# Optimization experiments

Measured on AMD Instinct MI355X. Metric: run time of the kernel, lower is better.

The kernel has to match this reference:

```python
import jax, jax.numpy as jnp
import numpy as np

DRN = 0.4
TWO_PI = 2.0 * np.pi


def _mlp(x, ws, bs):
    # torch_geometric MLP with act='LeakyRelu' (slope 0.01), dropout=0 (eval), norm treated as identity (eval running stats)
    for w, b in zip(ws[:-1], bs[:-1]):
        x = jax.nn.leaky_relu(x @ w + b, 0.01)
    return x @ ws[-1] + bs[-1]


def _conv(x, ws, bs):
    # x: [B, N, F] = [pt, h..., ang_re, ang_im]. Dense masked equivalent of radius-graph EdgeConv.
    ang = x[..., -2:]
    d2 = jnp.sum((ang[:, :, None, :] - ang[:, None, :, :]) ** 2, -1)
    adj = (d2 <= DRN * DRN).astype(x.dtype)  # [B,N,N], i=target, j=source, self-loops included (radius ball)
    h = x[..., 1:-2]
    B, N, H = h.shape
    hi = jnp.broadcast_to(h[:, :, None, :], (B, N, N, H))
    hj = jnp.broadcast_to(h[:, None, :, :], (B, N, N, H))
    re, im = ang[..., 0], ang[..., 1]
    r2 = re * re + im * im
    nrm = jnp.maximum(jnp.sqrt(r2[:, :, None] * r2[:, None, :]), 1e-12)
    cos = (re[:, :, None] * re[:, None, :] + im[:, :, None] * im[:, None, :]) / nrm
    sin = (im[:, :, None] * re[:, None, :] - re[:, :, None] * im[:, None, :]) / nrm
    feat = jnp.concatenate([hi, hj, hj - hi, cos[..., None], sin[..., None]], -1)
    m = _mlp(feat, ws, bs)  # [B,N,N,H_out+1]
    # pt-weighted aggregation: message pt is the TARGET's pt (x_i[:, :1] in torch code)
    pt = x[..., 0]
    msg_pt = pt[:, :, None] * adj
    denom = jnp.sum(msg_pt, -1, keepdims=True)
    w = jnp.where(denom > 0, msg_pt / denom, 0.0)  # nan_to_num equivalent
    agg = jnp.einsum('bij,bijk->bik', w, m)
    sw = jnp.sum(w, -1)
    agg_pt = pt * sw                      # sum_j w * pt_i
    agg_ang = ang * sw[..., None]          # sum_j w * ang_i
    # phase renormalization: exp(2*pi*i*gamma) * (re + i*im)
    gamma = agg[..., -1]
    c, s = jnp.cos(TWO_PI * gamma), jnp.sin(TWO_PI * gamma)
    re2 = c * agg_ang[..., 0] - s * agg_ang[..., 1]
    im2 = s * agg_ang[..., 0] + c * agg_ang[..., 1]
    return jnp.concatenate([agg_pt[..., None], agg[..., :-1], re2[..., None], im2[..., None]], -1)


def _forward(pt, angles, c0w, c0b, c1w, c1b, rw, rb):
    absz = jnp.sqrt(jnp.sum(angles ** 2, -1))  # |view_as_complex(angles)|
    x = jnp.concatenate([pt[..., None], absz[..., None], angles], -1)
    x = _conv(x, c0w, c0b)
    x = _conv(x, c1w, c1b)
    # pt-weighted readout over particles
    ptf = x[..., 0]
    denom = jnp.sum(ptf, -1, keepdims=True)
    wj = jnp.where(denom > 0, ptf / denom, 0.0)
    xg = jnp.einsum('bn,bnf->bf', wj, x[..., 1:])
    logits = _mlp(xg[:, :-2], rw, rb)
    return jnp.concatenate([jax.nn.sigmoid(logits), xg[:, -2:]], -1)


def setup_inputs() -> dict:
    key = jax.random.key(0)
    ks = jax.random.split(key, 16)
    B, N = 128, 128
    pt = jax.random.uniform(ks[0], (B, N), jnp.float32, 0.05, 1.0)  # all > 0 so mask is all-true
    angles = 0.25 * jax.random.normal(ks[1], (B, N, 2), jnp.float32)

    def lin(k, i, o):
        return (0.2 / np.sqrt(i)) * jax.random.normal(k, (i, o), jnp.float32) * np.sqrt(i)

    H = 16
    return {
        'pt': pt, 'angles': angles,
        'c0_w0': lin(ks[2], 5, H), 'c0_b0': jnp.zeros((H,), jnp.float32),
        'c0_w1': lin(ks[3], H, H + 1), 'c0_b1': jnp.zeros((H + 1,), jnp.float32),
        'c1_w0': lin(ks[4], 3 * H + 2, H), 'c1_b0': jnp.zeros((H,), jnp.float32),
        'c1_w1': lin(ks[5], H, H + 1), 'c1_b1': jnp.zeros((H + 1,), jnp.float32),
        'r_w0': lin(ks[6], H, 32), 'r_b0': jnp.zeros((32,), jnp.float32),
        'r_w1': lin(ks[7], 32, 32), 'r_b1': jnp.zeros((32,), jnp.float32),
        'r_w2': lin(ks[8], 32, 1), 'r_b2': jnp.zeros((1,), jnp.float32),
    }


def reference(pt, angles, c0_w0, c0_b0, c0_w1, c0_b1, c1_w0, c1_b0, c1_w1, c1_b1, r_w0, r_b0, r_w1, r_b1, r_w2, r_b2):
    return _forward(pt, angles, (c0_w0, c0_w1), (c0_b0, c0_b1), (c1_w0, c1_w1), (c1_b0, c1_b1), (r_w0, r_w1, r_w2), (r_b0, r_b1, r_b2))
```

## Files before the change

### kernel.cpp

```cpp
#include <hip/hip_runtime.h>
#include <math.h>


#define BB 128
#define NN 128
#define BN (BB * NN)

typedef float f32x2 __attribute__((ext_vector_type(2)));

__device__ __forceinline__ f32x2 pk2(float s) { f32x2 r; r[0] = s; r[1] = s; return r; }
__device__ __forceinline__ f32x2 pkfma(f32x2 a, f32x2 b, f32x2 c) {
    return __builtin_elementwise_fma(a, b, c);
}
__device__ __forceinline__ f32x2 pkmax(f32x2 a, f32x2 b) {
    return __builtin_elementwise_max(a, b);
}

template <int CTRL>
__device__ __forceinline__ float dpp_add(float x) {
    int tmp = __builtin_amdgcn_update_dpp(0, __float_as_int(x), CTRL, 0xF, 0xF, true);
    return x + __int_as_float(tmp);
}

__device__ __forceinline__ float grp16_sum(float x) {
    x = dpp_add<0xB1>(x);
    x = dpp_add<0x4E>(x);
    x = dpp_add<0x114>(x);
    x = dpp_add<0x118>(x);
    return x;
}

__device__ __forceinline__ float bcast_grp(float x, int bidx) {
    return __int_as_float(__builtin_amdgcn_ds_bpermute(bidx, __float_as_int(x)));
}

__global__ __launch_bounds__(256) void conv0_kernel(
    const float* __restrict__ ang,
    const float* __restrict__ w0,
    const float* __restrict__ b0,
    const float* __restrict__ w1,
    const float* __restrict__ b1,
    const float* __restrict__ nw0,
    const float* __restrict__ nb0,
    float* __restrict__ ang1,
    float* __restrict__ u1,
    float* __restrict__ v1)
{
    const int tid  = threadIdx.x;
    const int lane = tid & 63;
    const int wid  = tid >> 6;
    const int t    = lane & 15;
    const int g    = lane >> 4;
    const int ni   = blockIdx.x * 16 + wid * 4 + g;
    const int base = (blockIdx.x >> 3) << 7;

    __shared__ float hls[16][17];

    const float2 ai = ((const float2*)ang)[ni];
    const float r2i = fmaf(ai.x, ai.x, ai.y * ai.y);
    const float abszi = __builtin_amdgcn_sqrtf(r2i);
    const float invi  = __builtin_amdgcn_rsqf(r2i);

    f32x2 u0b2[8], q02[8], wc2[8], ws2[8];
    #pragma unroll
    for (int p = 0; p < 8; ++p) {
        f32x2 wa  = *(const f32x2*)(w0 + 2 * p);
        f32x2 wb  = *(const f32x2*)(w0 + 16 + 2 * p);
        f32x2 wcv = *(const f32x2*)(w0 + 32 + 2 * p);
        f32x2 bb  = *(const f32x2*)(b0 + 2 * p);
        u0b2[p] = pkfma(pk2(abszi), wa - wcv, bb);
        q02[p]  = wb + wcv;
        wc2[p]  = *(const f32x2*)(w0 + 48 + 2 * p);
        ws2[p]  = *(const f32x2*)(w0 + 64 + 2 * p);
    }

    float w1row[16], w1g[16];
    #pragma unroll
    for (int k = 0; k < 16; ++k) {
        w1row[k] = w1[k * 17 + t];
        w1g[k]   = w1[k * 17 + 16];
    }
    const float b1t = b1[t], b1g = b1[16];

    const int o   = lane & 31;
    const int kk  = o & 15;
    const bool isU = (o < 16);
    float wk[16];
    {
        const int off = isU ? 0 : 256;
        #pragma unroll
        for (int c = 0; c < 16; ++c) {
            float a_ = nw0[off + c * 16 + kk];
            float c_ = nw0[512 + c * 16 + kk];
            wk[c] = isU ? (a_ - c_) : (a_ + c_);
        }
    }
    const float accb = isU ? nb0[kk] : 0.0f;

    f32x2 A2[8];
    #pragma unroll
    for (int p = 0; p < 8; ++p) A2[p] = pk2(0.0f);
    float degf = 0.0f;

    #pragma unroll 4
    for (int jj = 0; jj < 8; ++jj) {
        const float2 aj = ((const float2*)ang)[base + jj * 16 + t];
        const float r2j = fmaf(aj.x, aj.x, aj.y * aj.y);
        const float abszj = __builtin_amdgcn_sqrtf(r2j);
        const float ivj   = __builtin_amdgcn_rsqf(r2j);
        const float dre = ai.x - aj.x, dim = ai.y - aj.y;
        const float d2 = fmaf(dre, dre, dim * dim);
        const float adjf = (d2 <= 0.16f) ? 1.0f : 0.0f;
        degf += adjf;
        const float inv = fminf(invi * ivj, 1e12f);
        const f32x2 cos2 = pk2(fmaf(ai.x, aj.x, ai.y * aj.y) * inv);
        const f32x2 sin2 = pk2(fmaf(ai.y, aj.x, -(ai.x * aj.y)) * inv);
        const f32x2 ab2 = pk2(abszj);
        const f32x2 adj2 = pk2(adjf);
        #pragma unroll
        for (int p = 0; p < 8; ++p) {
            f32x2 z = pkfma(ab2, q02[p], u0b2[p]);
            z = pkfma(cos2, wc2[p], z);
            z = pkfma(sin2, ws2[p], z);
            f32x2 a = pkmax(z, z * 0.01f);
            A2[p] = pkfma(a, adj2, A2[p]);
        }
    }

    const int bidx = (lane | 15) << 2;
    float Ak[16];
    #pragma unroll
    for (int p = 0; p < 8; ++p) {
        Ak[2 * p]     = bcast_grp(grp16_sum(A2[p][0]), bidx);
        Ak[2 * p + 1] = bcast_grp(grp16_sum(A2[p][1]), bidx);
    }
    const float degA = bcast_grp(grp16_sum(degf), bidx);
    const float invdeg = __builtin_amdgcn_rcpf(degA);

    float s = 0.0f, sg = 0.0f;
    #pragma unroll
    for (int k = 0; k < 16; ++k) {
        s  = fmaf(Ak[k], w1row[k], s);
        sg = fmaf(Ak[k], w1g[k], sg);
    }
    const float mt    = fmaf(s, invdeg, b1t);
    const float gamma = fmaf(sg, invdeg, b1g);

    {
        const float gf = gamma - floorf(gamma);
        const float cs = __builtin_amdgcn_cosf(gf);
        const float sn = __builtin_amdgcn_sinf(gf);
        const float re2 = cs * ai.x - sn * ai.y;
        const float im2 = fmaf(sn, ai.x, cs * ai.y);
        if (t == 0) ((float4*)ang1)[ni] = make_float4(re2, im2, invi, 0.0f);
    }

    hls[wid * 4 + g][t] = mt;

    #pragma unroll
    for (int p = 0; p < 2; ++p) {
        const int nl = (lane >> 5) + 2 * p;
        const int node = wid * 4 + nl;
        float acc = accb;
        #pragma unroll
        for (int c = 0; c < 16; ++c) acc = fmaf(hls[node][c], wk[c], acc);
        const int nig = blockIdx.x * 16 + nl;
        const int nout = (blockIdx.x * 16 + node);
        (void)nig;
        if (isU) u1[nout * 16 + kk] = acc;
        else     v1[nout * 16 + kk] = acc;
    }
}

__global__ __launch_bounds__(256) void conv1_kernel(
    const float* __restrict__ pt,
    const float* __restrict__ ang1,
    const float* __restrict__ u1,
    const float* __restrict__ v1,
    const float* __restrict__ w0,
    const float* __restrict__ w1,
    const float* __restrict__ b1,
    float* __restrict__ part)
{
    const int tid  = threadIdx.x;
    const int lane = tid & 63;
    const int wid  = tid >> 6;
    const int t    = lane & 15;
    const int g    = lane >> 4;
    const int ni   = blockIdx.x * 16 + wid * 4 + g;
    const int base = (blockIdx.x >> 3) << 7;

    const float4 a4 = ((const float4*)ang1)[ni];
    const float rei = a4.x, imi = a4.y, invi = a4.z;
    const float ptf = pt[ni];

    f32x2 u0b2[8], wc2[8], ws2[8];
    {
        const float4* ug = (const float4*)(u1 + (size_t)ni * 16);
        float4 q0 = ug[0], q1 = ug[1], q2 = ug[2], q3 = ug[3];
        u0b2[0][0] = q0.x; u0b2[0][1] = q0.y; u0b2[1][0] = q0.z; u0b2[1][1] = q0.w;
        u0b2[2][0] = q1.x; u0b2[2][1] = q1.y; u0b2[3][0] = q1.z; u0b2[3][1] = q1.w;
        u0b2[4][0] = q2.x; u0b2[4][1] = q2.y; u0b2[5][0] = q2.z; u0b2[5][1] = q2.w;
        u0b2[6][0] = q3.x; u0b2[6][1] = q3.y; u0b2[7][0] = q3.z; u0b2[7][1] = q3.w;
    }
    #pragma unroll
    for (int p = 0; p < 8; ++p) {
        wc2[p] = *(const f32x2*)(w0 + 768 + 2 * p);
        ws2[p] = *(const f32x2*)(w0 + 784 + 2 * p);
    }

    float w1row[16], w1g[16];
    #pragma unroll
    for (int k = 0; k < 16; ++k) {
        w1row[k] = w1[k * 17 + t];
        w1g[k]   = w1[k * 17 + 16];
    }
    const float b1t = b1[t], b1g = b1[16];

    f32x2 A2[8];
    #pragma unroll
    for (int p = 0; p < 8; ++p) A2[p] = pk2(0.0f);
    float degf = 0.0f;

    #pragma unroll 4
    for (int jj = 0; jj < 8; ++jj) {
        const int j = base + jj * 16 + t;
        const float4 aj = ((const float4*)ang1)[j];
        f32x2 vj2[8];
        {
            const float4* vg = (const float4*)(v1 + (size_t)j * 16);
            float4 q0 = vg[0], q1 = vg[1], q2 = vg[2], q3 = vg[3];
            vj2[0][0] = q0.x; vj2[0][1] = q0.y; vj2[1][0] = q0.z; vj2[1][1] = q0.w;
            vj2[2][0] = q1.x; vj2[2][1] = q1.y; vj2[3][0] = q1.z; vj2[3][1] = q1.w;
            vj2[4][0] = q2.x; vj2[4][1] = q2.y; vj2[5][0] = q2.z; vj2[5][1] = q2.w;
            vj2[6][0] = q3.x; vj2[6][1] = q3.y; vj2[7][0] = q3.z; vj2[7][1] = q3.w;
        }
        const float dre = rei - aj.x, dim = imi - aj.y;
        const float d2 = fmaf(dre, dre, dim * dim);
        const float adjf = (d2 <= 0.16f) ? 1.0f : 0.0f;
        degf += adjf;
        const float inv = fminf(invi * aj.z, 1e12f);
        const f32x2 cos2 = pk2(fmaf(rei, aj.x, imi * aj.y) * inv);
        const f32x2 sin2 = pk2(fmaf(imi, aj.x, -(rei * aj.y)) * inv);
        const f32x2 adj2 = pk2(adjf);
        #pragma unroll
        for (int p = 0; p < 8; ++p) {
            f32x2 z = u0b2[p] + vj2[p];
            z = pkfma(cos2, wc2[p], z);
            z = pkfma(sin2, ws2[p], z);
            f32x2 a = pkmax(z, z * 0.01f);
            A2[p] = pkfma(a, adj2, A2[p]);
        }
    }

    const int bidx = (lane | 15) << 2;
    float Ak[16];
    #pragma unroll
    for (int p = 0; p < 8; ++p) {
        Ak[2 * p]     = bcast_grp(grp16_sum(A2[p][0]), bidx);
        Ak[2 * p + 1] = bcast_grp(grp16_sum(A2[p][1]), bidx);
    }
    const float degA = bcast_grp(grp16_sum(degf), bidx);
    const float invdeg = __builtin_amdgcn_rcpf(degA);

    float s = 0.0f, sg = 0.0f;
    #pragma unroll
    for (int k = 0; k < 16; ++k) {
        s  = fmaf(Ak[k], w1row[k], s);
        sg = fmaf(Ak[k], w1g[k], sg);
    }
    const float mt    = fmaf(s, invdeg, b1t);
    const float gamma = fmaf(sg, invdeg, b1g);

    const float gf = gamma - floorf(gamma);
    const float cs = __builtin_amdgcn_cosf(gf);
    const float sn = __builtin_amdgcn_sinf(gf);
    const float re2 = cs * rei - sn * imi;
    const float im2 = fmaf(sn, rei, cs * imi);

    float pm  = ptf * mt;
    float pre = ptf * re2;
    float pim = ptf * im2;
    float ppt = ptf;
    pm  += __int_as_float(__builtin_amdgcn_ds_swizzle(__float_as_int(pm),  0x401F));
    pre += __int_as_float(__builtin_amdgcn_ds_swizzle(__float_as_int(pre), 0x401F));
    pim += __int_as_float(__builtin_amdgcn_ds_swizzle(__float_as_int(pim), 0x401F));
    ppt += __int_as_float(__builtin_amdgcn_ds_swizzle(__float_as_int(ppt), 0x401F));
    pm  += __shfl_xor(pm, 32);
    pre += __shfl_xor(pre, 32);
    pim += __shfl_xor(pim, 32);
    ppt += __shfl_xor(ppt, 32);

    float* po = part + (size_t)(blockIdx.x * 4 + wid) * 20;
    if (lane < 16)       po[lane] = pm;
    else if (lane == 16) po[16] = pre;
    else if (lane == 17) po[17] = pim;
    else if (lane == 18) po[18] = ppt;
}

__global__ __launch_bounds__(64) void readout_kernel(
    const float* __restrict__ part,
    const float* __restrict__ w0, const float* __restrict__ b0,
    const float* __restrict__ w1, const float* __restrict__ b1,
    const float* __restrict__ w2, const float* __restrict__ b2,
    float* __restrict__ out) {
    const int b = blockIdx.x;
    const int t = threadIdx.x;

    __shared__ float sbuf[19];
    __shared__ float xg[18];
    __shared__ float h1r[32];

    if (t < 19) {
        float s0 = 0.0f, s1 = 0.0f, s2 = 0.0f, s3 = 0.0f;
        const float* pb = part + (size_t)b * 32 * 20 + t;
        #pragma unroll
        for (int r = 0; r < 32; r += 4) {
            s0 += pb[(r + 0) * 20];
            s1 += pb[(r + 1) * 20];
            s2 += pb[(r + 2) * 20];
            s3 += pb[(r + 3) * 20];
        }
        sbuf[t] = (s0 + s1) + (s2 + s3);
    }
    const float invd = __builtin_amdgcn_rcpf(sbuf[18]);
    if (t < 18) xg[t] = sbuf[t] * invd;

    if (t < 32) {
        float h = b0[t];
        #pragma unroll
        for (int k = 0; k < 16; ++k) h = fmaf(xg[k], w0[k * 32 + t], h);
        h = fmaxf(h, 0.01f * h);
        h1r[t] = h;
    }
    if (t < 32) {
        float h = b1[t];
        #pragma unroll
        for (int k = 0; k < 32; ++k) h = fmaf(h1r[k], w1[k * 32 + t], h);
        h = fmaxf(h, 0.01f * h);
        float p = h * w2[t];
        #pragma unroll
        for (int off = 16; off; off >>= 1) p += __shfl_xor(p, off);
        if (t == 0) {
            out[b * 3 + 0] = 1.0f / (1.0f + expf(-(p + b2[0])));
            out[b * 3 + 1] = xg[16];
            out[b * 3 + 2] = xg[17];
        }
    }
}

extern "C" void kernel_launch(void* const* d_in, const int* in_sizes, int n_in,
                              void* d_out, int out_size, void* d_ws, size_t ws_size,
                              hipStream_t stream) {
    const float* pt    = (const float*)d_in[0];
    const float* ang   = (const float*)d_in[1];
    const float* c0_w0 = (const float*)d_in[2];
    const float* c0_b0 = (const float*)d_in[3];
    const float* c0_w1 = (const float*)d_in[4];
    const float* c0_b1 = (const float*)d_in[5];
    const float* c1_w0 = (const float*)d_in[6];
    const float* c1_b0 = (const float*)d_in[7];
    const float* c1_w1 = (const float*)d_in[8];
    const float* c1_b1 = (const float*)d_in[9];
    const float* r_w0  = (const float*)d_in[10];
    const float* r_b0  = (const float*)d_in[11];
    const float* r_w1  = (const float*)d_in[12];
    const float* r_b1  = (const float*)d_in[13];
    const float* r_w2  = (const float*)d_in[14];
    const float* r_b2  = (const float*)d_in[15];
    float* out = (float*)d_out;
    float* ws = (float*)d_ws;

    float* ang1  = ws;
    float* u1    = ang1 + (size_t)BN * 4;
    float* v1    = u1 + (size_t)BN * 16;
    float* partb = v1 + (size_t)BN * 16;

    hipLaunchKernelGGL(conv0_kernel, dim3(BN / 16), dim3(256), 0, stream,
                       ang, c0_w0, c0_b0, c0_w1, c0_b1, c1_w0, c1_b0,
                       ang1, u1, v1);
    hipLaunchKernelGGL(conv1_kernel, dim3(BN / 16), dim3(256), 0, stream,
                       pt, ang1, u1, v1, c1_w0, c1_w1, c1_b1, partb);
    hipLaunchKernelGGL(readout_kernel, dim3(BB), dim3(64), 0, stream,
                       partb, r_w0, r_b0, r_w1, r_b1, r_w2, r_b2, out);
}
```

Before: 30.21 us.

## Prefetch neighbour loads, store unit vectors, pack FMAs, add occupancy bounds

Conv0 now loads all neighbour angles up front and fully unrolls its loop. It stores normalised unit vectors (rotated by the phase) so conv1 computes cos/sin directly without the per-edge inverse-norm multiply. Conv1 software-pipelines the neighbour record and v1 loads three steps ahead, and both kernels defer weight loads, use packed FMAs for the final matvecs, and set launch_bounds min-blocks to 4. This trades register pressure and a slight change in rounding for better latency hiding and fewer ALU ops.

```diff
diff --git a/kernel.cpp b/kernel.cpp
--- a/kernel.cpp
+++ b/kernel.cpp
@@ -34,7 +34,14 @@
     return __int_as_float(__builtin_amdgcn_ds_bpermute(bidx, __float_as_int(x)));
 }
 
-__global__ __launch_bounds__(256) void conv0_kernel(
+__device__ __forceinline__ f32x2 grp16_red2(f32x2 x, int bidx) {
+    f32x2 r;
+    r[0] = bcast_grp(grp16_sum(x[0]), bidx);
+    r[1] = bcast_grp(grp16_sum(x[1]), bidx);
+    return r;
+}
+
+__global__ __launch_bounds__(256, 4) void conv0_kernel(
     const float* __restrict__ ang,
     const float* __restrict__ w0,
     const float* __restrict__ b0,
@@ -42,24 +49,29 @@
     const float* __restrict__ b1,
     const float* __restrict__ nw0,
     const float* __restrict__ nb0,
-    float* __restrict__ ang1,
+    float* __restrict__ rec,
     float* __restrict__ u1,
     float* __restrict__ v1)
 {
-    const int tid  = threadIdx.x;
-    const int lane = tid & 63;
-    const int wid  = tid >> 6;
+    const int lane = threadIdx.x & 63;
+    const int wid  = threadIdx.x >> 6;
     const int t    = lane & 15;
     const int g    = lane >> 4;
     const int ni   = blockIdx.x * 16 + wid * 4 + g;
     const int base = (blockIdx.x >> 3) << 7;
 
-    __shared__ float hls[16][17];
+    __shared__ float hls[16][20];
 
     const float2 ai = ((const float2*)ang)[ni];
     const float r2i = fmaf(ai.x, ai.x, ai.y * ai.y);
     const float abszi = __builtin_amdgcn_sqrtf(r2i);
-    const float invi  = __builtin_amdgcn_rsqf(r2i);
+    const float ivi = fminf(__builtin_amdgcn_rsqf(r2i), 1e12f);
+    const float eix = ai.x * ivi, eiy = ai.y * ivi;
+
+    float2 ajv[8];
+    #pragma unroll
+    for (int jj = 0; jj < 8; ++jj)
+        ajv[jj] = ((const float2*)ang)[base + jj * 16 + t];
 
     f32x2 u0b2[8], q02[8], wc2[8], ws2[8];
     #pragma unroll
@@ -74,47 +86,24 @@
         ws2[p]  = *(const f32x2*)(w0 + 64 + 2 * p);
     }
 
-    float w1row[16], w1g[16];
-    #pragma unroll
-    for (int k = 0; k < 16; ++k) {
-        w1row[k] = w1[k * 17 + t];
-        w1g[k]   = w1[k * 17 + 16];
-    }
-    const float b1t = b1[t], b1g = b1[16];
-
-    const int o   = lane & 31;
-    const int kk  = o & 15;
-    const bool isU = (o < 16);
-    float wk[16];
-    {
-        const int off = isU ? 0 : 256;
-        #pragma unroll
-        for (int c = 0; c < 16; ++c) {
-            float a_ = nw0[off + c * 16 + kk];
-            float c_ = nw0[512 + c * 16 + kk];
-            wk[c] = isU ? (a_ - c_) : (a_ + c_);
-        }
-    }
-    const float accb = isU ? nb0[kk] : 0.0f;
-
     f32x2 A2[8];
     #pragma unroll
     for (int p = 0; p < 8; ++p) A2[p] = pk2(0.0f);
     float degf = 0.0f;
 
-    #pragma unroll 4
+    #pragma unroll
     for (int jj = 0; jj < 8; ++jj) {
-        const float2 aj = ((const float2*)ang)[base + jj * 16 + t];
+        const float2 aj = ajv[jj];
         const float r2j = fmaf(aj.x, aj.x, aj.y * aj.y);
         const float abszj = __builtin_amdgcn_sqrtf(r2j);
-        const float ivj   = __builtin_amdgcn_rsqf(r2j);
+        const float ivj = fminf(__builtin_amdgcn_rsqf(r2j), 1e12f);
+        const float ejx = aj.x * ivj, ejy = aj.y * ivj;
         const float dre = ai.x - aj.x, dim = ai.y - aj.y;
         const float d2 = fmaf(dre, dre, dim * dim);
         const float adjf = (d2 <= 0.16f) ? 1.0f : 0.0f;
         degf += adjf;
-        const float inv = fminf(invi * ivj, 1e12f);
-        const f32x2 cos2 = pk2(fmaf(ai.x, aj.x, ai.y * aj.y) * inv);
-        const f32x2 sin2 = pk2(fmaf(ai.y, aj.x, -(ai.x * aj.y)) * inv);
+        const f32x2 cos2 = pk2(fmaf(eix, ejx, eiy * ejy));
+        const f32x2 sin2 = pk2(fmaf(eiy, ejx, -(eix * ejy)));
         const f32x2 ab2 = pk2(abszj);
         const f32x2 adj2 = pk2(adjf);
         #pragma unroll
@@ -128,53 +117,76 @@
     }
 
     const int bidx = (lane | 15) << 2;
-    float Ak[16];
+    f32x2 Ak2[8];
+    #pragma unroll
+    for (int p = 0; p < 8; ++p) Ak2[p] = grp16_red2(A2[p], bidx);
+    const float invdeg = __builtin_amdgcn_rcpf(bcast_grp(grp16_sum(degf), bidx));
+
+    f32x2 s2 = pk2(0.0f), g2 = pk2(0.0f);
     #pragma unroll
     for (int p = 0; p < 8; ++p) {
-        Ak[2 * p]     = bcast_grp(grp16_sum(A2[p][0]), bidx);
-        Ak[2 * p + 1] = bcast_grp(grp16_sum(A2[p][1]), bidx);
-    }
-    const float degA = bcast_grp(grp16_sum(degf), bidx);
-    const float invdeg = __builtin_amdgcn_rcpf(degA);
-
-    float s = 0.0f, sg = 0.0f;
-    #pragma unroll
-    for (int k = 0; k < 16; ++k) {
-        s  = fmaf(Ak[k], w1row[k], s);
-        sg = fmaf(Ak[k], w1g[k], sg);
-    }
-    const float mt    = fmaf(s, invdeg, b1t);
-    const float gamma = fmaf(sg, invdeg, b1g);
+        f32x2 wr; wr[0] = w1[(2 * p) * 17 + t];  wr[1] = w1[(2 * p + 1) * 17 + t];
+        f32x2 wg; wg[0] = w1[(2 * p) * 17 + 16]; wg[1] = w1[(2 * p + 1) * 17 + 16];
+        s2 = pkfma(Ak2[p], wr, s2);
+        g2 = pkfma(Ak2[p], wg, g2);
+    }
+    const float mt    = fmaf(s2[0] + s2[1], invdeg, b1[t]);
+    const float gamma = fmaf(g2[0] + g2[1], invdeg, b1[16]);
 
     {
         const float gf = gamma - floorf(gamma);
         const float cs = __builtin_amdgcn_cosf(gf);
         const float sn = __builtin_amdgcn_sinf(gf);
-        const float re2 = cs * ai.x - sn * ai.y;
-        const float im2 = fmaf(sn, ai.x, cs * ai.y);
-        if (t == 0) ((float4*)ang1)[ni] = make_float4(re2, im2, invi, 0.0f);
+        if (t == 0) {
+            const float re2 = cs * ai.x - sn * ai.y;
+            const float im2 = fmaf(sn, ai.x, cs * ai.y);
+            const float e1x = cs * eix - sn * eiy;
+            const float e1y = fmaf(sn, eix, cs * eiy);
+            ((float4*)rec)[ni] = make_float4(re2, im2, e1x, e1y);
+        }
     }
 
     hls[wid * 4 + g][t] = mt;
 
-    #pragma unroll
-    for (int p = 0; p < 2; ++p) {
-        const int nl = (lane >> 5) + 2 * p;
+    const int o = lane & 31;
+    const int kk = o & 15;
+    const bool isU = (o < 16);
+    const float accb = isU ? nb0[kk] : 0.0f;
+    f32x2 wk2[8];
+    {
+        const int off = isU ? 0 : 256;
+        const float sgn = isU ? -1.0f : 1.0f;
+        #pragma unroll
+        for (int p = 0; p < 8; ++p) {
+            f32x2 a_; a_[0] = nw0[off + (2 * p) * 16 + kk]; a_[1] = nw0[off + (2 * p + 1) * 16 + kk];
+            f32x2 c_; c_[0] = nw0[512 + (2 * p) * 16 + kk]; c_[1] = nw0[512 + (2 * p + 1) * 16 + kk];
+            wk2[p] = pkfma(pk2(sgn), c_, a_);
+        }
+    }
+    #pragma unroll
+    for (int ps = 0; ps < 2; ++ps) {
+        const int nl = (lane >> 5) + 2 * ps;
         const int node = wid * 4 + nl;
-        float acc = accb;
-        #pragma unroll
-        for (int c = 0; c < 16; ++c) acc = fmaf(hls[node][c], wk[c], acc);
-        const int nig = blockIdx.x * 16 + nl;
-        const int nout = (blockIdx.x * 16 + node);
-        (void)nig;
+        const float4* hr = (const float4*)&hls[node][0];
+        float4 h0 = hr[0], h1 = hr[1], h2 = hr[2], h3 = hr[3];
+        f32x2 hv[8];
+        hv[0][0] = h0.x; hv[0][1] = h0.y; hv[1][0] = h0.z; hv[1][1] = h0.w;
+        hv[2][0] = h1.x; hv[2][1] = h1.y; hv[3][0] = h1.z; hv[3][1] = h1.w;
+        hv[4][0] = h2.x; hv[4][1] = h2.y; hv[5][0] = h2.z; hv[5][1] = h2.w;
+        hv[6][0] = h3.x; hv[6][1] = h3.y; hv[7][0] = h3.z; hv[7][1] = h3.w;
+        f32x2 acc2 = pk2(0.0f);
+        #pragma unroll
+        for (int p = 0; p < 8; ++p) acc2 = pkfma(hv[p], wk2[p], acc2);
+        const float acc = acc2[0] + acc2[1] + accb;
+        const int nout = blockIdx.x * 16 + node;
         if (isU) u1[nout * 16 + kk] = acc;
         else     v1[nout * 16 + kk] = acc;
     }
 }
 
-__global__ __launch_bounds__(256) void conv1_kernel(
+__global__ __launch_bounds__(256, 4) void conv1_kernel(
     const float* __restrict__ pt,
-    const float* __restrict__ ang1,
+    const float* __restrict__ rec,
     const float* __restrict__ u1,
     const float* __restrict__ v1,
     const float* __restrict__ w0,
@@ -182,19 +194,17 @@
     const float* __restrict__ b1,
     float* __restrict__ part)
 {
-    const int tid  = threadIdx.x;
-    const int lane = tid & 63;
-    const int wid  = tid >> 6;
+    const int lane = threadIdx.x & 63;
+    const int wid  = threadIdx.x >> 6;
     const int t    = lane & 15;
     const int g    = lane >> 4;
     const int ni   = blockIdx.x * 16 + wid * 4 + g;
     const int base = (blockIdx.x >> 3) << 7;
 
-    const float4 a4 = ((const float4*)ang1)[ni];
-    const float rei = a4.x, imi = a4.y, invi = a4.z;
+    const float4 r4i = ((const float4*)rec)[ni];
+    const float rei = r4i.x, imi = r4i.y, eix = r4i.z, eiy = r4i.w;
     const float ptf = pt[ni];
-
-    f32x2 u0b2[8], wc2[8], ws2[8];
+    f32x2 u0b2[8];
     {
         const float4* ug = (const float4*)(u1 + (size_t)ni * 16);
         float4 q0 = ug[0], q1 = ug[1], q2 = ug[2], q3 = ug[3];
@@ -203,74 +213,72 @@
         u0b2[4][0] = q2.x; u0b2[4][1] = q2.y; u0b2[5][0] = q2.z; u0b2[5][1] = q2.w;
         u0b2[6][0] = q3.x; u0b2[6][1] = q3.y; u0b2[7][0] = q3.z; u0b2[7][1] = q3.w;
     }
+    f32x2 wc2[8], ws2[8];
     #pragma unroll
     for (int p = 0; p < 8; ++p) {
         wc2[p] = *(const f32x2*)(w0 + 768 + 2 * p);
         ws2[p] = *(const f32x2*)(w0 + 784 + 2 * p);
     }
 
-    float w1row[16], w1g[16];
-    #pragma unroll
-    for (int k = 0; k < 16; ++k) {
-        w1row[k] = w1[k * 17 + t];
-        w1g[k]   = w1[k * 17 + 16];
-    }
-    const float b1t = b1[t], b1g = b1[16];
-
     f32x2 A2[8];
     #pragma unroll
     for (int p = 0; p < 8; ++p) A2[p] = pk2(0.0f);
     float degf = 0.0f;
 
-    #pragma unroll 4
-    for (int jj = 0; jj < 8; ++jj) {
-        const int j = base + jj * 16 + t;
-        const float4 aj = ((const float4*)ang1)[j];
-        f32x2 vj2[8];
-        {
-            const float4* vg = (const float4*)(v1 + (size_t)j * 16);
-            float4 q0 = vg[0], q1 = vg[1], q2 = vg[2], q3 = vg[3];
-            vj2[0][0] = q0.x; vj2[0][1] = q0.y; vj2[1][0] = q0.z; vj2[1][1] = q0.w;
-            vj2[2][0] = q1.x; vj2[2][1] = q1.y; vj2[3][0] = q1.z; vj2[3][1] = q1.w;
-            vj2[4][0] = q2.x; vj2[4][1] = q2.y; vj2[5][0] = q2.z; vj2[5][1] = q2.w;
-            vj2[6][0] = q3.x; vj2[6][1] = q3.y; vj2[7][0] = q3.z; vj2[7][1] = q3.w;
-        }
-        const float dre = rei - aj.x, dim = imi - aj.y;
-        const float d2 = fmaf(dre, dre, dim * dim);
-        const float adjf = (d2 <= 0.16f) ? 1.0f : 0.0f;
-        degf += adjf;
-        const float inv = fminf(invi * aj.z, 1e12f);
-        const f32x2 cos2 = pk2(fmaf(rei, aj.x, imi * aj.y) * inv);
-        const f32x2 sin2 = pk2(fmaf(imi, aj.x, -(rei * aj.y)) * inv);
-        const f32x2 adj2 = pk2(adjf);
-        #pragma unroll
-        for (int p = 0; p < 8; ++p) {
-            f32x2 z = u0b2[p] + vj2[p];
-            z = pkfma(cos2, wc2[p], z);
-            z = pkfma(sin2, ws2[p], z);
-            f32x2 a = pkmax(z, z * 0.01f);
-            A2[p] = pkfma(a, adj2, A2[p]);
-        }
-    }
+    float4 pa[3], pv0[3], pv1[3], pv2[3], pv3[3];
+#define LJ(slot, jj) { const int j_ = base + (jj) * 16 + t;                     \
+        pa[slot] = ((const float4*)rec)[j_];                                    \
+        const float4* vg_ = (const float4*)(v1 + (size_t)j_ * 16);              \
+        pv0[slot] = vg_[0]; pv1[slot] = vg_[1];                                 \
+        pv2[slot] = vg_[2]; pv3[slot] = vg_[3]; }
+#define STEP(jj, slot, pf)                                                      \
+    {   const float4 r4 = pa[slot];                                             \
+        const float4 q0 = pv0[slot], q1 = pv1[slot], q2 = pv2[slot], q3 = pv3[slot]; \
+        if (pf) LJ(slot, (jj) + 3);                                             \
+        f32x2 vj2[8];                                                           \
+        vj2[0][0] = q0.x; vj2[0][1] = q0.y; vj2[1][0] = q0.z; vj2[1][1] = q0.w; \
+        vj2[2][0] = q1.x; vj2[2][1] = q1.y; vj2[3][0] = q1.z; vj2[3][1] = q1.w; \
+        vj2[4][0] = q2.x; vj2[4][1] = q2.y; vj2[5][0] = q2.z; vj2[5][1] = q2.w; \
+        vj2[6][0] = q3.x; vj2[6][1] = q3.y; vj2[7][0] = q3.z; vj2[7][1] = q3.w; \
+        const float dre = rei - r4.x, dim = imi - r4.y;                         \
+        const float d2 = fmaf(dre, dre, dim * dim);                             \
+        const float adjf = (d2 <= 0.16f) ? 1.0f : 0.0f;                         \
+        degf += adjf;                                                           \
+        const f32x2 cos2 = pk2(fmaf(eix, r4.z, eiy * r4.w));                    \
+        const f32x2 sin2 = pk2(fmaf(eiy, r4.z, -(eix * r4.w)));                 \
+        const f32x2 adj2 = pk2(adjf);                                           \
+        _Pragma("unroll")                                                       \
+        for (int p = 0; p < 8; ++p) {                                           \
+            f32x2 z = u0b2[p] + vj2[p];                                         \
+            z = pkfma(cos2, wc2[p], z);                                         \
+            z = pkfma(sin2, ws2[p], z);                                         \
+            f32x2 a = pkmax(z, z * 0.01f);                                      \
+            A2[p] = pkfma(a, adj2, A2[p]);                                      \
+        }                                                                       \
+    }
+
+    LJ(0, 0); LJ(1, 1); LJ(2, 2);
+    STEP(0, 0, 1); STEP(1, 1, 1); STEP(2, 2, 1); STEP(3, 0, 1); STEP(4, 1, 1);
+    STEP(5, 2, 0); STEP(6, 0, 0); STEP(7, 1, 0);
+#undef STEP
+#undef LJ
 
     const int bidx = (lane | 15) << 2;
-    float Ak[16];
+    f32x2 Ak2[8];
+    #pragma unroll
+    for (int p = 0; p < 8; ++p) Ak2[p] = grp16_red2(A2[p], bidx);
+    const float invdeg = __builtin_amdgcn_rcpf(bcast_grp(grp16_sum(degf), bidx));
+
+    f32x2 s2 = pk2(0.0f), g2 = pk2(0.0f);
     #pragma unroll
     for (int p = 0; p < 8; ++p) {
-        Ak[2 * p]     = bcast_grp(grp16_sum(A2[p][0]), bidx);
-        Ak[2 * p + 1] = bcast_grp(grp16_sum(A2[p][1]), bidx);
-    }
-    const float degA = bcast_grp(grp16_sum(degf), bidx);
-    const float invdeg = __builtin_amdgcn_rcpf(degA);
-
-    float s = 0.0f, sg = 0.0f;
-    #pragma unroll
-    for (int k = 0; k < 16; ++k) {
-        s  = fmaf(Ak[k], w1row[k], s);
-        sg = fmaf(Ak[k], w1g[k], sg);
-    }
-    const float mt    = fmaf(s, invdeg, b1t);
-    const float gamma = fmaf(sg, invdeg, b1g);
+        f32x2 wr; wr[0] = w1[(2 * p) * 17 + t];  wr[1] = w1[(2 * p + 1) * 17 + t];
+        f32x2 wg; wg[0] = w1[(2 * p) * 17 + 16]; wg[1] = w1[(2 * p + 1) * 17 + 16];
+        s2 = pkfma(Ak2[p], wr, s2);
+        g2 = pkfma(Ak2[p], wg, g2);
+    }
+    const float mt    = fmaf(s2[0] + s2[1], invdeg, b1[t]);
+    const float gamma = fmaf(g2[0] + g2[1], invdeg, b1[16]);
 
     const float gf = gamma - floorf(gamma);
     const float cs = __builtin_amdgcn_cosf(gf);
@@ -371,16 +379,16 @@
     float* out = (float*)d_out;
     float* ws = (float*)d_ws;
 
-    float* ang1  = ws;
-    float* u1    = ang1 + (size_t)BN * 4;
+    float* recb  = ws;
+    float* u1    = recb + (size_t)BN * 4;
     float* v1    = u1 + (size_t)BN * 16;
     float* partb = v1 + (size_t)BN * 16;
 
     hipLaunchKernelGGL(conv0_kernel, dim3(BN / 16), dim3(256), 0, stream,
                        ang, c0_w0, c0_b0, c0_w1, c0_b1, c1_w0, c1_b0,
-                       ang1, u1, v1);
+                       recb, u1, v1);
     hipLaunchKernelGGL(conv1_kernel, dim3(BN / 16), dim3(256), 0, stream,
-                       pt, ang1, u1, v1, c1_w0, c1_w1, c1_b1, partb);
+                       pt, recb, u1, v1, c1_w0, c1_w1, c1_b1, partb);
     hipLaunchKernelGGL(readout_kernel, dim3(BB), dim3(64), 0, stream,
                        partb, r_w0, r_b0, r_w1, r_b1, r_w2, r_b2, out);
 }
```

New measurement: 41.23 us. 36.5% more time.
